# Kernel tuning notes

Hardware: AMD Instinct MI355X
Metric: run time of the kernel (lower is better)

## Reference

```python
import jax, jax.numpy as jnp
import numpy as np

N, E, G = 2048, 4096, 128      # nodes, edges, graphs
H, IN, ED = 128, 11, 4         # hidden, input node feat, edge feat
BN_EPS = 1e-5


def setup_inputs() -> dict:
    key = jax.random.key(0)
    ks = iter(jax.random.split(key, 40))
    r = lambda shape, s=0.1: jax.random.normal(next(ks), shape, jnp.float32) * s
    inp = dict(
        x=r((N, IN), 1.0),
        edge_attr=jax.random.uniform(next(ks), (E, ED), jnp.float32),
        edge_index=jax.random.randint(next(ks), (2, E), 0, N).astype(jnp.int32),
        batch=jnp.sort(jax.random.randint(next(ks), (N,), 0, G)).astype(jnp.int32),
        # layer 0 (in=11 -> out=128)
        w1_0=r((ED, H)), b1_0=jnp.zeros(H), w2_0=r((H, IN * H), 0.02), b2_0=jnp.zeros(IN * H),
        root_0=r((IN, H)), bias_0=jnp.zeros(H),
        bn_g0=jnp.ones(H), bn_b0=jnp.zeros(H), bn_m0=r((H,), 0.1),
        bn_v0=jax.random.uniform(next(ks), (H,), jnp.float32, 0.5, 1.5),
        # layers 1..4 stacked (in=out=128)
        w1_s=r((4, ED, H)), b1_s=jnp.zeros((4, H)), w2_s=r((4, H, H * H), 0.02), b2_s=jnp.zeros((4, H * H)),
        root_s=r((4, H, H)), bias_s=jnp.zeros((4, H)),
        bn_gs=jnp.ones((4, H)), bn_bs=jnp.zeros((4, H)), bn_ms=r((4, H), 0.1),
        bn_vs=jax.random.uniform(next(ks), (4, H), jnp.float32, 0.5, 1.5),
        # readout MLP
        lin1_w=r((H, H // 2)), lin1_b=jnp.zeros(H // 2),
        lin2_w=r((H // 2, 1)), lin2_b=jnp.zeros(1),
    )
    return inp


def _nnconv(x, src, dst, edge_attr, w1, b1, w2, b2, root, bias):
    in_c = x.shape[-1]
    h = jax.nn.relu(edge_attr @ w1 + b1)                 # [E, H]
    w_e = (h @ w2 + b2).reshape(-1, in_c, H)             # [E, in, H] per-edge weight
    msg = jnp.einsum('ei,eio->eo', x[src], w_e)          # gather + per-edge matvec
    s = jax.ops.segment_sum(msg, dst, num_segments=N)
    cnt = jax.ops.segment_sum(jnp.ones(dst.shape, x.dtype), dst, num_segments=N)
    aggr = s / jnp.maximum(cnt, 1.0)[:, None]            # scatter-mean
    return aggr + x @ root + bias


def _bn_eval(x, g, b, m, v):
    return (x - m) * jax.lax.rsqrt(v + BN_EPS) * g + b


def reference(x, edge_attr, w1_0, b1_0, w2_0, b2_0, root_0, bias_0,
              bn_g0, bn_b0, bn_m0, bn_v0,
              w1_s, b1_s, w2_s, b2_s, root_s, bias_s,
              bn_gs, bn_bs, bn_ms, bn_vs,
              lin1_w, lin1_b, lin2_w, lin2_b,
              edge_index, batch):
    src, dst = edge_index[0], edge_index[1]
    # layer 0
    h = jax.nn.relu(_bn_eval(
        _nnconv(x, src, dst, edge_attr, w1_0, b1_0, w2_0, b2_0, root_0, bias_0),
        bn_g0, bn_b0, bn_m0, bn_v0))
    # layers 1..4 with residual (dims match)
    for l in range(4):
        h_new = jax.nn.relu(_bn_eval(
            _nnconv(h, src, dst, edge_attr, w1_s[l], b1_s[l], w2_s[l], b2_s[l], root_s[l], bias_s[l]),
            bn_gs[l], bn_bs[l], bn_ms[l], bn_vs[l]))
        h = h + h_new
    # global mean pool over graphs
    gs = jax.ops.segment_sum(h, batch, num_segments=G)
    gc = jax.ops.segment_sum(jnp.ones((N,), h.dtype), batch, num_segments=G)
    g = gs / jnp.maximum(gc, 1.0)[:, None]
    # readout (dropout is identity in eval mode)
    g = jax.nn.relu(g @ lin1_w + lin1_b)
    return g @ lin2_w + lin2_b
```

## Files before the change

### kernel.cpp

```cpp
#include <hip/hip_runtime.h>
#include <cstdint>
#include <cstddef>

#define NN 2048
#define NE 4096
#define NG 128
#define HD 128
#define SKM 16
#define SK0 5
#define NCH 64
#define CHE 64

typedef __attribute__((ext_vector_type(8))) _Float16 f16x8;
typedef __attribute__((ext_vector_type(4))) float f32x4;

#define GLOAD_LDS16(gptr, lptr)                                                          \
  __builtin_amdgcn_global_load_lds((const __attribute__((address_space(1))) unsigned int*)(gptr), \
                                   (__attribute__((address_space(3))) unsigned int*)(lptr), 16, 0, 0)

__global__ __launch_bounds__(256) void k_prep(
    const float* __restrict__ ea,
    const float* __restrict__ w1_0, const float* __restrict__ b1_0,
    const float* __restrict__ w1_s, const float* __restrict__ b1_s,
    const float* __restrict__ x,
    const float* __restrict__ w2_0, const float* __restrict__ b2_0,
    const float* __restrict__ w2s, const float* __restrict__ b2s,
    const int* __restrict__ dst, int* __restrict__ hist,
    _Float16* __restrict__ hb, _Float16* __restrict__ x16,
    _Float16* __restrict__ w2T0, _Float16* __restrict__ w2T) {
  __shared__ float sld[64][65];
  const int bid = blockIdx.x, t = threadIdx.x;

  if (bid < 10240) {
    int idx = bid * 256 + t;
    int c = idx & (HD - 1);
    int e = (idx >> 7) & (NE - 1);
    int l = idx >> 19;
    const float* w1 = (l == 0) ? w1_0 : (w1_s + (size_t)(l - 1) * 4 * HD);
    const float* b1 = (l == 0) ? b1_0 : (b1_s + (size_t)(l - 1) * HD);
    float4 a = *(const float4*)(ea + (size_t)e * 4);
    float v = b1[c] + a.x * w1[c] + a.y * w1[HD + c] + a.z * w1[2 * HD + c] + a.w * w1[3 * HD + c];
    hb[idx] = (_Float16)fmaxf(v, 0.f);
  } else if (bid < 10368) {
    int idx = (bid - 10240) * 256 + t;
    int n = idx >> 4, i = idx & 15;
    x16[idx] = (_Float16)(i < 11 ? x[(size_t)n * 11 + i] : 0.f);
  } else if (bid < 10496) {
    int o = bid - 10368;
    for (int kap = t; kap < 2080; kap += 256) {
      int k = kap >> 4, i = kap & 15;
      float v = 0.f;
      if (i < 11) {
        if (k < 128) v = w2_0[(size_t)k * 1408 + i * 128 + o];
        else if (k == 128) v = b2_0[i * 128 + o];
      }
      w2T0[(size_t)o * 2080 + kap] = (_Float16)v;
    }
  } else if (bid < 12560) {
    int idx2 = bid - 10496;
    int l = idx2 / 516;
    int rem = idx2 - l * 516;
    int ob = rem / 258;
    int kb = rem - ob * 258;
    const float* w2 = w2s + (size_t)l * 16384 * 128;
    const float* b2 = b2s + (size_t)l * 128 * 128;
    _Float16* outp = w2T + (size_t)l * 128 * 16512;
    int k0 = kb * 64, o0 = ob * 64;
    int r = t >> 4, c4 = (t & 15) * 4;
#pragma unroll
    for (int it = 0; it < 4; ++it) {
      int kk = k0 + r + it * 16;
      const float* srcp = (kk < 16384) ? (w2 + (size_t)kk * 128 + o0 + c4)
                                       : (b2 + (size_t)(kk - 16384) * 128 + o0 + c4);
      *(float4*)&sld[r + it * 16][c4] = *(const float4*)srcp;
    }
    __syncthreads();
    int rr = t >> 3, c8 = (t & 7) * 8;
#pragma unroll
    for (int it = 0; it < 2; ++it) {
      int ol = rr + it * 32;
      _Float16 pk[8];
#pragma unroll
      for (int j = 0; j < 8; ++j) pk[j] = (_Float16)sld[c8 + j][ol];
      *(f16x8*)(outp + (size_t)(o0 + ol) * 16512 + k0 + c8) = *(const f16x8*)pk;
    }
  } else {
    int e = (bid - 12560) * 256 + t;
    if (e < NE) atomicAdd(&hist[(e >> 6) * NN + dst[e]], 1);
  }
}

__global__ __launch_bounds__(1024) void k_scan2(const int* __restrict__ hist,
                                                int* __restrict__ rowptr,
                                                int* __restrict__ chunkoff,
                                                const int* __restrict__ batch,
                                                int* __restrict__ gstart) {
  __shared__ int s[NN];
  int t = threadIdx.x;
  int c0 = 0, c1 = 0;
  for (int c = 0; c < NCH; ++c) { c0 += hist[c * NN + t]; c1 += hist[c * NN + t + 1024]; }
  s[t] = c0; s[t + 1024] = c1;
  __syncthreads();
  for (int d = 1; d < NN; d <<= 1) {
    int a0 = s[t], a1 = s[t + 1024];
    int v0 = (t >= d) ? s[t - d] : 0;
    int v1 = (t + 1024 >= d) ? s[t + 1024 - d] : 0;
    __syncthreads();
    s[t] = a0 + v0; s[t + 1024] = a1 + v1;
    __syncthreads();
  }
  rowptr[t + 1] = s[t]; rowptr[t + 1025] = s[t + 1024];
  if (t == 0) rowptr[0] = 0;
  int run0 = s[t] - c0, run1 = s[t + 1024] - c1;
  for (int c = 0; c < NCH; ++c) {
    chunkoff[c * NN + t] = run0;        run0 += hist[c * NN + t];
    chunkoff[c * NN + t + 1024] = run1; run1 += hist[c * NN + t + 1024];
  }
  if (t <= NG) {
    int lo = 0, hi = NN;
    while (lo < hi) { int mid = (lo + hi) >> 1; if (batch[mid] < t) lo = mid + 1; else hi = mid; }
    gstart[t] = lo;
  }
}

__global__ __launch_bounds__(64) void k_fill2(const int* __restrict__ dst,
                                              const int* __restrict__ chunkoff,
                                              int* __restrict__ elist) {
  __shared__ int sd[CHE];
  int c = blockIdx.x, t = threadIdx.x;
  int e = c * CHE + t;
  int dv = dst[e];
  sd[t] = dv;
  __syncthreads();
  int lrank = 0;
  for (int j = 0; j < t; ++j) lrank += (sd[j] == dv) ? 1 : 0;
  elist[chunkoff[c * NN + dv] + lrank] = e;
}

__global__ __launch_bounds__(256, 2) void k_mma0(
    const _Float16* __restrict__ xh,
    const _Float16* __restrict__ hb,
    const _Float16* __restrict__ w2T,
    const int* __restrict__ src,
    _Float16* __restrict__ msgp) {
  constexpr int KT = 2080;
  __shared__ _Float16 Bs[2][4096];
  __shared__ _Float16 hTl[26][128];

  const int tid = threadIdx.x;
  const int e0 = blockIdx.x * 128;
  const int w = tid >> 6, l = tid & 63, l16 = l & 15, g = l >> 4;

  const int k0 = blockIdx.y * 13, nk = 13;
  const int kb = k0 * 2;

  int nd[8];
#pragma unroll
  for (int mt = 0; mt < 8; ++mt) nd[mt] = src[e0 + mt * 16 + l16];

  for (int idx = tid; idx < 26 * 128; idx += 256) {
    int kk = idx >> 7, m = idx & 127;
    int k = kb + kk;
    _Float16 v;
    if (k < 128) v = hb[(size_t)(e0 + m) * 128 + k];
    else v = (k == 128) ? (_Float16)1.0f : (_Float16)0.0f;
    hTl[kk][m] = v;
  }

  f16x8 xr[8];
#pragma unroll
  for (int mt = 0; mt < 8; ++mt)
    xr[mt] = *(const f16x8*)(xh + (size_t)nd[mt] * 16 + (g & 1) * 8);

  auto stageB = [&](int buf, int c) {
    const int kap0 = c * 32;
#pragma unroll
    for (int j2 = 0; j2 < 2; ++j2) {
      int ntg = w * 2 + j2;
      const _Float16* gp = w2T + (size_t)(ntg * 16 + l16) * KT + kap0 + g * 8;
      GLOAD_LDS16(gp, &Bs[buf][(w * 128 + j2 * 64) * 8]);
    }
  };

  stageB(0, k0);
  __syncthreads();

  f32x4 acc[8][2];
#pragma unroll
  for (int mt = 0; mt < 8; ++mt)
#pragma unroll
    for (int jj = 0; jj < 2; ++jj) acc[mt][jj] = (f32x4){0.f, 0.f, 0.f, 0.f};

  int buf = 0;
  for (int j = 0; j < nk; ++j) {
    if (j + 1 < nk) {
      stageB(buf ^ 1, k0 + j + 1);
      asm volatile("s_waitcnt vmcnt(2)" ::: "memory");
    } else {
      asm volatile("s_waitcnt vmcnt(0)" ::: "memory");
    }
    __builtin_amdgcn_sched_barrier(0);

    f16x8 bv0 = *(const f16x8*)&Bs[buf][(size_t)(w * 2 + 0) * 512 + l * 8];
    f16x8 bv1 = *(const f16x8*)&Bs[buf][(size_t)(w * 2 + 1) * 512 + l * 8];
#pragma unroll
    for (int mt = 0; mt < 8; ++mt) {
      _Float16 hh = hTl[2 * j + (g >> 1)][mt * 16 + l16];
      f16x8 hv = {hh, hh, hh, hh, hh, hh, hh, hh};
      f16x8 av = xr[mt] * hv;
      acc[mt][0] = __builtin_amdgcn_mfma_f32_16x16x32_f16(av, bv0, acc[mt][0], 0, 0, 0);
      acc[mt][1] = __builtin_amdgcn_mfma_f32_16x16x32_f16(av, bv1, acc[mt][1], 0, 0, 0);
    }
    buf ^= 1;
    __syncthreads();
  }

  _Float16* mp = msgp + ((size_t)blockIdx.y * NE + e0) * 128;
#pragma unroll
  for (int mt = 0; mt < 8; ++mt)
#pragma unroll
    for (int jj = 0; jj < 2; ++jj)
#pragma unroll
      for (int r = 0; r < 4; ++r) {
        int row = mt * 16 + 4 * g + r;
        mp[(size_t)row * 128 + w * 32 + jj * 16 + l16] = (_Float16)acc[mt][jj][r];
      }
}

__global__ __launch_bounds__(512, 2) void k_mma3(
    const _Float16* __restrict__ xh,
    const _Float16* __restrict__ hb,
    const _Float16* __restrict__ w2T,
    const int* __restrict__ src,
    _Float16* __restrict__ msgp) {
  constexpr int KT = 16512;
  __shared__ __align__(16) _Float16 Bs[4][4096];
  __shared__ _Float16 hTl[9][256];

  const int tid = threadIdx.x;
  const int w = tid >> 6, l = tid & 63, l16 = l & 15, g = l >> 4;
  const int bid = blockIdx.x;
  const int eb = bid >> 4, sk = bid & 15;
  const int e0 = eb * 256;
  const int mg = w & 3, ng = w >> 2;

  int k0, nk;
  if (sk == 0) { k0 = 0; nk = 9; } else { k0 = 9 + (sk - 1) * 8; nk = 8; }
  const int nsteps = nk * 4;

  auto stageB = [&](int s) {
    const int jk = s >> 2, win = s & 3;
    const int kap0 = (k0 + jk) * 128 + win * 32;
    const _Float16* gp = w2T + (size_t)(w * 16 + l16) * KT + kap0 + g * 8;
    GLOAD_LDS16(gp, &Bs[s & 3][w * 512]);
  };

  stageB(0);
  stageB(1);

  int nd[4];
#pragma unroll
  for (int mt = 0; mt < 4; ++mt) nd[mt] = src[e0 + mg * 64 + mt * 16 + l16];
  f16x8 xw[4][4];
#pragma unroll
  for (int mt = 0; mt < 4; ++mt)
#pragma unroll
    for (int win = 0; win < 4; ++win)
      xw[mt][win] = *(const f16x8*)(xh + (size_t)nd[mt] * 128 + win * 32 + g * 8);

  for (int idx = tid; idx < nk * 256; idx += 512) {
    int jk = idx >> 8, m = idx & 255;
    int k = k0 + jk;
    hTl[jk][m] = (k < 128) ? hb[(size_t)(e0 + m) * 128 + k]
                           : (_Float16)(k == 128 ? 1.0f : 0.0f);
  }
  __syncthreads();

  f32x4 acc[4][4];
#pragma unroll
  for (int mt = 0; mt < 4; ++mt)
#pragma unroll
    for (int j2 = 0; j2 < 4; ++j2) acc[mt][j2] = (f32x4){0.f, 0.f, 0.f, 0.f};

  for (int jk = 0; jk < nk; ++jk) {
    _Float16 hv[4];
#pragma unroll
    for (int mt = 0; mt < 4; ++mt) hv[mt] = hTl[jk][mg * 64 + mt * 16 + l16];
#pragma unroll
    for (int win = 0; win < 4; ++win) {
      const int s = jk * 4 + win;
      if (s + 2 < nsteps) {
        stageB(s + 2);
        asm volatile("s_waitcnt vmcnt(2)" ::: "memory");
      } else if (s + 2 == nsteps) {
        asm volatile("s_waitcnt vmcnt(1)" ::: "memory");
      } else {
        asm volatile("s_waitcnt vmcnt(0)" ::: "memory");
      }
      __builtin_amdgcn_s_barrier();

      const _Float16* bp = &Bs[win][ng * 2048 + g * 128 + l16 * 8];
      f16x8 bv0 = *(const f16x8*)(bp);
      f16x8 bv1 = *(const f16x8*)(bp + 512);
      f16x8 bv2 = *(const f16x8*)(bp + 1024);
      f16x8 bv3 = *(const f16x8*)(bp + 1536);
#pragma unroll
      for (int mt = 0; mt < 4; ++mt) {
        _Float16 hh = hv[mt];
        f16x8 hs = {hh, hh, hh, hh, hh, hh, hh, hh};
        f16x8 av = xw[mt][win] * hs;
        acc[mt][0] = __builtin_amdgcn_mfma_f32_16x16x32_f16(av, bv0, acc[mt][0], 0, 0, 0);
        acc[mt][1] = __builtin_amdgcn_mfma_f32_16x16x32_f16(av, bv1, acc[mt][1], 0, 0, 0);
        acc[mt][2] = __builtin_amdgcn_mfma_f32_16x16x32_f16(av, bv2, acc[mt][2], 0, 0, 0);
        acc[mt][3] = __builtin_amdgcn_mfma_f32_16x16x32_f16(av, bv3, acc[mt][3], 0, 0, 0);
      }
    }
  }

  _Float16* mp = msgp + ((size_t)sk * NE + e0) * 128;
#pragma unroll
  for (int mt = 0; mt < 4; ++mt)
#pragma unroll
    for (int j2 = 0; j2 < 4; ++j2)
#pragma unroll
      for (int r = 0; r < 4; ++r) {
        int row = mg * 64 + mt * 16 + 4 * g + r;
        int col = (ng * 4 + j2) * 16 + l16;
        mp[(size_t)row * 128 + col] = (_Float16)acc[mt][j2][r];
      }
}

template <int NSK>
__global__ __launch_bounds__(256) void k_msum(const _Float16* __restrict__ msgp,
                                              float* __restrict__ msgf) {
  int idx = blockIdx.x * 256 + threadIdx.x;
  const _Float16* p = msgp + (size_t)idx * 8;
  float s0 = 0.f, s1 = 0.f, s2 = 0.f, s3 = 0.f, s4 = 0.f, s5 = 0.f, s6 = 0.f, s7 = 0.f;
#pragma unroll
  for (int k = 0; k < NSK; ++k) {
    f16x8 v = *(const f16x8*)(p + (size_t)k * NE * HD);
    s0 += (float)v[0]; s1 += (float)v[1]; s2 += (float)v[2]; s3 += (float)v[3];
    s4 += (float)v[4]; s5 += (float)v[5]; s6 += (float)v[6]; s7 += (float)v[7];
  }
  float4* o = (float4*)(msgf + (size_t)idx * 8);
  o[0] = (float4){s0, s1, s2, s3};
  o[1] = (float4){s4, s5, s6, s7};
}

template <int INR>
__global__ void k_au(const float* __restrict__ msgf, const int* __restrict__ rowptr,
                     const int* __restrict__ elist, const float* __restrict__ xin,
                     const float* __restrict__ root, const float* __restrict__ bias,
                     const float* __restrict__ bg, const float* __restrict__ bb,
                     const float* __restrict__ bm, const float* __restrict__ bv,
                     const float* __restrict__ h_prev, float* __restrict__ h_out,
                     _Float16* __restrict__ h_out_h) {
  int n = blockIdx.x, t = threadIdx.x;
  __shared__ float xr[INR];
  if (t < INR) xr[t] = xin[(size_t)n * INR + t];
  int beg = rowptr[n], end = rowptr[n + 1];
  float v = 0.f;
  for (int j = beg; j < end; ++j) v += msgf[(size_t)elist[j] * HD + t];
  v /= fmaxf((float)(end - beg), 1.f);
  __syncthreads();
  float acc = v + bias[t];
  if constexpr (INR == 128) {
    float a0 = 0.f, a1 = 0.f, a2 = 0.f, a3 = 0.f;
#pragma unroll 4
    for (int k = 0; k < 128; k += 4) {
      a0 += xr[k + 0] * root[(size_t)(k + 0) * HD + t];
      a1 += xr[k + 1] * root[(size_t)(k + 1) * HD + t];
      a2 += xr[k + 2] * root[(size_t)(k + 2) * HD + t];
      a3 += xr[k + 3] * root[(size_t)(k + 3) * HD + t];
    }
    acc += (a0 + a1) + (a2 + a3);
  } else {
#pragma unroll
    for (int k = 0; k < INR; ++k) acc += xr[k] * root[(size_t)k * HD + t];
  }
  float bn = (acc - bm[t]) * rsqrtf(bv[t] + 1e-5f) * bg[t] + bb[t];
  float r = fmaxf(bn, 0.f);
  float val = h_prev ? (h_prev[(size_t)n * HD + t] + r) : r;
  h_out[(size_t)n * HD + t] = val;
  h_out_h[(size_t)n * HD + t] = (_Float16)val;
}

__global__ void k_poolread(const float* __restrict__ h, const int* __restrict__ gstart,
                           const float* __restrict__ w1, const float* __restrict__ b1,
                           const float* __restrict__ w2, const float* __restrict__ b2,
                           float* __restrict__ out) {
  int g = blockIdx.x, t = threadIdx.x;
  __shared__ float row[HD];
  int beg = gstart[g], end = gstart[g + 1];
  float v = 0.f;
  for (int n = beg; n < end; ++n) v += h[(size_t)n * HD + t];
  row[t] = v / fmaxf((float)(end - beg), 1.f);
  __syncthreads();
  if (t < 64) {
    float acc = b1[t];
#pragma unroll 8
    for (int k = 0; k < HD; ++k) acc += row[k] * w1[(size_t)k * 64 + t];
    float vv = fmaxf(acc, 0.f) * w2[t];
#pragma unroll
    for (int off = 32; off > 0; off >>= 1) vv += __shfl_down(vv, off);
    if (t == 0) out[g] = vv + b2[0];
  }
}

extern "C" void kernel_launch(void* const* d_in, const int* in_sizes, int n_in,
                              void* d_out, int out_size, void* d_ws, size_t ws_size,
                              hipStream_t stream) {
  const float* x      = (const float*)d_in[0];
  const float* ea     = (const float*)d_in[1];
  const int*   eidx   = (const int*)d_in[2];
  const int*   batch  = (const int*)d_in[3];
  const float* w1_0   = (const float*)d_in[4];
  const float* b1_0   = (const float*)d_in[5];
  const float* w2_0   = (const float*)d_in[6];
  const float* b2_0   = (const float*)d_in[7];
  const float* root_0 = (const float*)d_in[8];
  const float* bias_0 = (const float*)d_in[9];
  const float* bn_g0  = (const float*)d_in[10];
  const float* bn_b0  = (const float*)d_in[11];
  const float* bn_m0  = (const float*)d_in[12];
  const float* bn_v0  = (const float*)d_in[13];
  const float* w1_s   = (const float*)d_in[14];
  const float* b1_s   = (const float*)d_in[15];
  const float* w2_s   = (const float*)d_in[16];
  const float* b2_s   = (const float*)d_in[17];
  const float* root_s = (const float*)d_in[18];
  const float* bias_s = (const float*)d_in[19];
  const float* bn_gs  = (const float*)d_in[20];
  const float* bn_bs  = (const float*)d_in[21];
  const float* bn_ms  = (const float*)d_in[22];
  const float* bn_vs  = (const float*)d_in[23];
  const float* lin1_w = (const float*)d_in[24];
  const float* lin1_b = (const float*)d_in[25];
  const float* lin2_w = (const float*)d_in[26];
  const float* lin2_b = (const float*)d_in[27];
  float* out = (float*)d_out;

  char* wsb = (char*)d_ws;
  size_t off = 0;
  auto alloc = [&](size_t bytes) { void* p = wsb + off; off = (off + bytes + 255) & ~(size_t)255; return p; };
  int*      rowptr   = (int*)alloc((NN + 4) * 4);
  int*      elist    = (int*)alloc(NE * 4);
  int*      gstart   = (int*)alloc((NG + 4) * 4);
  int*      hist     = (int*)alloc((size_t)NCH * NN * 4);
  int*      chunkoff = (int*)alloc((size_t)NCH * NN * 4);
  _Float16* hbf      = (_Float16*)alloc((size_t)5 * NE * HD * 2);
  _Float16* x16      = (_Float16*)alloc((size_t)NN * 16 * 2);
  _Float16* w2T0     = (_Float16*)alloc((size_t)128 * 2080 * 2);
  _Float16* w2T      = (_Float16*)alloc((size_t)4 * 128 * 16512 * 2);
  float*    hnA      = (float*)alloc((size_t)NN * HD * 4);
  float*    hnB      = (float*)alloc((size_t)NN * HD * 4);
  _Float16* hnAh     = (_Float16*)alloc((size_t)NN * HD * 2);
  _Float16* hnBh     = (_Float16*)alloc((size_t)NN * HD * 2);
  _Float16* msgp     = (_Float16*)alloc((size_t)SKM * NE * HD * 2);
  float*    msgf     = (float*)alloc((size_t)NE * HD * 4);

  const int* src = eidx;
  const int* dstp = eidx + NE;

  hipMemsetAsync(hist, 0, (size_t)NCH * NN * 4, stream);
  k_prep<<<dim3(12576), 256, 0, stream>>>(ea, w1_0, b1_0, w1_s, b1_s, x,
                                          w2_0, b2_0, w2_s, b2_s,
                                          dstp, hist, hbf, x16, w2T0, w2T);
  k_scan2<<<1, 1024, 0, stream>>>(hist, rowptr, chunkoff, batch, gstart);
  k_fill2<<<dim3(NCH), 64, 0, stream>>>(dstp, chunkoff, elist);

  k_mma0<<<dim3(NE / 128, SK0), 256, 0, stream>>>(x16, hbf, w2T0, src, msgp);
  k_msum<SK0><<<dim3(256), 256, 0, stream>>>(msgp, msgf);
  k_au<11><<<NN, HD, 0, stream>>>(msgf, rowptr, elist, x, root_0, bias_0,
                                  bn_g0, bn_b0, bn_m0, bn_v0, nullptr, hnA, hnAh);

  float* cur = hnA;  _Float16* curh = hnAh;
  float* nxt = hnB;  _Float16* nxth = hnBh;
  for (int l = 1; l <= 4; ++l) {
    const _Float16* w2Tl = w2T + (size_t)(l - 1) * 128 * 16512;
    k_mma3<<<dim3(256), 512, 0, stream>>>(curh, hbf + (size_t)l * NE * HD, w2Tl, src, msgp);
    k_msum<SKM><<<dim3(256), 256, 0, stream>>>(msgp, msgf);
    k_au<128><<<NN, HD, 0, stream>>>(msgf, rowptr, elist, cur,
                                     root_s + (size_t)(l - 1) * HD * HD,
                                     bias_s + (size_t)(l - 1) * HD,
                                     bn_gs + (size_t)(l - 1) * HD, bn_bs + (size_t)(l - 1) * HD,
                                     bn_ms + (size_t)(l - 1) * HD, bn_vs + (size_t)(l - 1) * HD,
                                     cur, nxt, nxth);
    float* tf = cur; cur = nxt; nxt = tf;
    _Float16* th = curh; curh = nxth; nxth = th;
  }

  k_poolread<<<NG, HD, 0, stream>>>(cur, gstart, lin1_w, lin1_b, lin2_w, lin2_b, out);
}
```

Measured before the change: 241.2 us.

## Retile per-edge MFMA kernel to 128-edge blocks with win-outer loop and double buffer

Replaces k_mma3 (256-edge tiles, 512 threads, 4-stage B ring, h values staged in LDS) with k_mma4. The new kernel uses 128-edge tiles, 256 threads and a 2-D grid of 32x16 blocks. The loop now iterates over 32-wide x windows on the outside and the 8 k-slices on the inside. Each lane keeps h values in registers loaded as an f16x8 vector, which removes the hTl LDS staging. The bias row is handled as an extra step on the last split-K block, and B staging is double-buffered with sched_barrier in place of s_barrier, which may shift the balance between occupancy and latency hiding.

```diff
diff --git a/kernel.cpp b/kernel.cpp
--- a/kernel.cpp
+++ b/kernel.cpp
@@ -227,106 +227,111 @@
       }
 }
 
-__global__ __launch_bounds__(512, 2) void k_mma3(
+__global__ __launch_bounds__(256, 2) void k_mma4(
     const _Float16* __restrict__ xh,
     const _Float16* __restrict__ hb,
     const _Float16* __restrict__ w2T,
     const int* __restrict__ src,
     _Float16* __restrict__ msgp) {
   constexpr int KT = 16512;
-  __shared__ __align__(16) _Float16 Bs[4][4096];
-  __shared__ _Float16 hTl[9][256];
+  __shared__ __align__(16) _Float16 Bs[2][4096];
 
   const int tid = threadIdx.x;
   const int w = tid >> 6, l = tid & 63, l16 = l & 15, g = l >> 4;
-  const int bid = blockIdx.x;
-  const int eb = bid >> 4, sk = bid & 15;
-  const int e0 = eb * 256;
-  const int mg = w & 3, ng = w >> 2;
-
-  int k0, nk;
-  if (sk == 0) { k0 = 0; nk = 9; } else { k0 = 9 + (sk - 1) * 8; nk = 8; }
-  const int nsteps = nk * 4;
-
-  auto stageB = [&](int s) {
-    const int jk = s >> 2, win = s & 3;
-    const int kap0 = (k0 + jk) * 128 + win * 32;
-    const _Float16* gp = w2T + (size_t)(w * 16 + l16) * KT + kap0 + g * 8;
-    GLOAD_LDS16(gp, &Bs[s & 3][w * 512]);
+  const int e0 = blockIdx.x * 128;
+  const int sk = blockIdx.y;
+  const int k0 = sk * 8;
+  const bool haveBias = (sk == 15);
+
+  int nd[8];
+#pragma unroll
+  for (int mt = 0; mt < 8; ++mt) nd[mt] = src[e0 + mt * 16 + l16];
+
+  f16x8 hv[8];
+#pragma unroll
+  for (int mt = 0; mt < 8; ++mt)
+    hv[mt] = *(const f16x8*)(hb + (size_t)(e0 + mt * 16 + l16) * 128 + k0);
+
+  auto stageB = [&](int buf, int kap0) {
+#pragma unroll
+    for (int j2 = 0; j2 < 2; ++j2) {
+      const _Float16* gp = w2T + (size_t)((w * 2 + j2) * 16 + l16) * KT + kap0 + g * 8;
+      GLOAD_LDS16(gp, &Bs[buf][(w * 2 + j2) * 512]);
+    }
   };
 
-  stageB(0);
-  stageB(1);
-
-  int nd[4];
-#pragma unroll
-  for (int mt = 0; mt < 4; ++mt) nd[mt] = src[e0 + mg * 64 + mt * 16 + l16];
-  f16x8 xw[4][4];
-#pragma unroll
-  for (int mt = 0; mt < 4; ++mt)
-#pragma unroll
-    for (int win = 0; win < 4; ++win)
-      xw[mt][win] = *(const f16x8*)(xh + (size_t)nd[mt] * 128 + win * 32 + g * 8);
-
-  for (int idx = tid; idx < nk * 256; idx += 512) {
-    int jk = idx >> 8, m = idx & 255;
-    int k = k0 + jk;
-    hTl[jk][m] = (k < 128) ? hb[(size_t)(e0 + m) * 128 + k]
-                           : (_Float16)(k == 128 ? 1.0f : 0.0f);
-  }
-  __syncthreads();
-
-  f32x4 acc[4][4];
-#pragma unroll
-  for (int mt = 0; mt < 4; ++mt)
-#pragma unroll
-    for (int j2 = 0; j2 < 4; ++j2) acc[mt][j2] = (f32x4){0.f, 0.f, 0.f, 0.f};
-
-  for (int jk = 0; jk < nk; ++jk) {
-    _Float16 hv[4];
-#pragma unroll
-    for (int mt = 0; mt < 4; ++mt) hv[mt] = hTl[jk][mg * 64 + mt * 16 + l16];
-#pragma unroll
-    for (int win = 0; win < 4; ++win) {
-      const int s = jk * 4 + win;
-      if (s + 2 < nsteps) {
-        stageB(s + 2);
+  f32x4 acc[8][2];
+#pragma unroll
+  for (int mt = 0; mt < 8; ++mt) {
+    acc[mt][0] = (f32x4){0.f, 0.f, 0.f, 0.f};
+    acc[mt][1] = (f32x4){0.f, 0.f, 0.f, 0.f};
+  }
+
+  int buf = 0;
+  stageB(0, k0 * 128);
+
+#define CONSUME(AV_EXPR)                                                              \
+  {                                                                                   \
+    f16x8 bv0 = *(const f16x8*)&Bs[buf][(w * 2 + 0) * 512 + l * 8];                   \
+    f16x8 bv1 = *(const f16x8*)&Bs[buf][(w * 2 + 1) * 512 + l * 8];                   \
+    _Pragma("unroll")                                                                 \
+    for (int mt = 0; mt < 8; ++mt) {                                                  \
+      f16x8 av = (AV_EXPR);                                                           \
+      acc[mt][0] = __builtin_amdgcn_mfma_f32_16x16x32_f16(av, bv0, acc[mt][0], 0, 0, 0); \
+      acc[mt][1] = __builtin_amdgcn_mfma_f32_16x16x32_f16(av, bv1, acc[mt][1], 0, 0, 0); \
+    }                                                                                 \
+    buf ^= 1;                                                                         \
+  }
+
+#pragma unroll
+  for (int win = 0; win < 4; ++win) {
+    f16x8 xw[8];
+#pragma unroll
+    for (int mt = 0; mt < 8; ++mt)
+      xw[mt] = *(const f16x8*)(xh + (size_t)nd[mt] * 128 + win * 32 + g * 8);
+
+#pragma unroll
+    for (int jk = 0; jk < 8; ++jk) {
+      if (jk < 7) {
+        stageB(buf ^ 1, (k0 + jk + 1) * 128 + win * 32);
         asm volatile("s_waitcnt vmcnt(2)" ::: "memory");
-      } else if (s + 2 == nsteps) {
-        asm volatile("s_waitcnt vmcnt(1)" ::: "memory");
+      } else if (haveBias) {
+        stageB(buf ^ 1, 16384 + win * 32);
+        asm volatile("s_waitcnt vmcnt(2)" ::: "memory");
+      } else if (win < 3) {
+        stageB(buf ^ 1, k0 * 128 + (win + 1) * 32);
+        asm volatile("s_waitcnt vmcnt(2)" ::: "memory");
       } else {
         asm volatile("s_waitcnt vmcnt(0)" ::: "memory");
       }
-      __builtin_amdgcn_s_barrier();
-
-      const _Float16* bp = &Bs[win][ng * 2048 + g * 128 + l16 * 8];
-      f16x8 bv0 = *(const f16x8*)(bp);
-      f16x8 bv1 = *(const f16x8*)(bp + 512);
-      f16x8 bv2 = *(const f16x8*)(bp + 1024);
-      f16x8 bv3 = *(const f16x8*)(bp + 1536);
-#pragma unroll
-      for (int mt = 0; mt < 4; ++mt) {
-        _Float16 hh = hv[mt];
-        f16x8 hs = {hh, hh, hh, hh, hh, hh, hh, hh};
-        f16x8 av = xw[mt][win] * hs;
-        acc[mt][0] = __builtin_amdgcn_mfma_f32_16x16x32_f16(av, bv0, acc[mt][0], 0, 0, 0);
-        acc[mt][1] = __builtin_amdgcn_mfma_f32_16x16x32_f16(av, bv1, acc[mt][1], 0, 0, 0);
-        acc[mt][2] = __builtin_amdgcn_mfma_f32_16x16x32_f16(av, bv2, acc[mt][2], 0, 0, 0);
-        acc[mt][3] = __builtin_amdgcn_mfma_f32_16x16x32_f16(av, bv3, acc[mt][3], 0, 0, 0);
+      __builtin_amdgcn_sched_barrier(0);
+      _Float16 hh;
+      CONSUME(({ hh = hv[mt][jk];
+                 f16x8 hs = {hh, hh, hh, hh, hh, hh, hh, hh};
+                 xw[mt] * hs; }));
+    }
+    if (haveBias) {
+      if (win < 3) {
+        stageB(buf ^ 1, k0 * 128 + (win + 1) * 32);
+        asm volatile("s_waitcnt vmcnt(2)" ::: "memory");
+      } else {
+        asm volatile("s_waitcnt vmcnt(0)" ::: "memory");
       }
-    }
-  }
+      __builtin_amdgcn_sched_barrier(0);
+      CONSUME((xw[mt]));
+    }
+  }
+#undef CONSUME
 
   _Float16* mp = msgp + ((size_t)sk * NE + e0) * 128;
 #pragma unroll
-  for (int mt = 0; mt < 4; ++mt)
-#pragma unroll
-    for (int j2 = 0; j2 < 4; ++j2)
+  for (int mt = 0; mt < 8; ++mt)
+#pragma unroll
+    for (int jj = 0; jj < 2; ++jj)
 #pragma unroll
       for (int r = 0; r < 4; ++r) {
-        int row = mg * 64 + mt * 16 + 4 * g + r;
-        int col = (ng * 4 + j2) * 16 + l16;
-        mp[(size_t)row * 128 + col] = (_Float16)acc[mt][j2][r];
+        int row = mt * 16 + 4 * g + r;
+        mp[(size_t)row * 128 + w * 32 + jj * 16 + l16] = (_Float16)acc[mt][jj][r];
       }
 }
 
@@ -478,7 +483,8 @@
   float* nxt = hnB;  _Float16* nxth = hnBh;
   for (int l = 1; l <= 4; ++l) {
     const _Float16* w2Tl = w2T + (size_t)(l - 1) * 128 * 16512;
-    k_mma3<<<dim3(256), 512, 0, stream>>>(curh, hbf + (size_t)l * NE * HD, w2Tl, src, msgp);
+    k_mma4<<<dim3(NE / 128, SKM), 256, 0, stream>>>(curh, hbf + (size_t)l * NE * HD,
+                                                    w2Tl, src, msgp);
     k_msum<SKM><<<dim3(256), 256, 0, stream>>>(msgp, msgf);
     k_au<128><<<NN, HD, 0, stream>>>(msgf, rowptr, elist, cur,
                                      root_s + (size_t)(l - 1) * HD * HD,
```

Measured after the change: 246.6 us. 1.02x slower.
